# Performance work log

Hardware: AMD Instinct MI355X
Metric: run time of the kernel (lower is better)

The kernel has to match this reference:

```python
import jax, jax.numpy as jnp
import numpy as np

MIN_MARGIN = 0.15
MAX_MARGIN = 0.6
NUM_CALLS = 1  # first call; margin anneals over 40000 calls in the original
MARGIN = min(MIN_MARGIN + float(NUM_CALLS) / 40000.0 * (MAX_MARGIN - MIN_MARGIN), MAX_MARGIN)

B, C, D = 8192, 20000, 128


def setup_inputs() -> dict:
    key = jax.random.key(0)
    k1, k2, k3 = jax.random.split(key, 3)
    features = jax.random.normal(k1, (B, D), dtype=jnp.float32)
    centers = jax.random.normal(k2, (C, D), dtype=jnp.float32)
    labels = jax.random.randint(k3, (B,), 0, C, dtype=jnp.int64)
    return {"features": features, "centers": centers, "labels": labels}


def reference(features, centers, labels):
    # L2-normalize features along dim 1 (F.normalize default, eps=1e-12)
    norm = jnp.linalg.norm(features, axis=1, keepdims=True)
    f = features / jnp.maximum(norm, 1e-12)

    batch_centers = centers[labels]                       # [B, D]
    pos_distances = 1.0 - jnp.sum(f * batch_centers, axis=1)   # [B]
    neg_distances = 1.0 - jnp.einsum('bd,cd->bc', f, centers)  # [B, C]

    losses = MARGIN + pos_distances[:, None] - neg_distances   # [B, C]

    center_ids = jnp.arange(C, dtype=labels.dtype)
    different_class = labels[:, None] != center_ids[None, :]   # [B, C] bool
    valid = (different_class & (losses > 0.0)).astype(jnp.float32)

    num_valid = jnp.sum(valid)
    total = jnp.sum(losses * valid)
    return jnp.where(num_valid > 0, total / num_valid, jnp.zeros((), dtype=losses.dtype))
```

## Files before the change

kernel.cpp:

```cpp
#include <hip/hip_runtime.h>

#define B_N 8192
#define C_N 20000
#define D_N 128
#define CPAD 20096
#define NPAD 96
#define NTILES32 628
#define NCHUNK 24
#define MARGIN_F 0.15001125f

#define NORM_BLOCKS 1024
#define CONV_BLOCKS 2512

typedef __attribute__((ext_vector_type(8))) short bf16x8;
typedef __attribute__((ext_vector_type(4))) float f32x4;

typedef __attribute__((address_space(1))) const unsigned int GUint;
typedef __attribute__((address_space(3))) unsigned int LUint;

__device__ __forceinline__ unsigned short f2bf(float x) {
    union { float f; unsigned int u; } v; v.f = x;
    unsigned int r = v.u + 0x7fffu + ((v.u >> 16) & 1u);
    return (unsigned short)(r >> 16);
}
__device__ __forceinline__ float bf2f(unsigned short h) {
    union { unsigned int u; float f; } v; v.u = ((unsigned int)h) << 16; return v.f;
}

__global__ __launch_bounds__(256) void k_prep(
    const float* __restrict__ feat, const float* __restrict__ centers,
    const int* __restrict__ labels, unsigned short* __restrict__ fb,
    unsigned short* __restrict__ cb, float* __restrict__ t,
    float* __restrict__ corr_s, unsigned int* __restrict__ corr_c)
{
    const int bid = blockIdx.x;
    if (bid < NORM_BLOCKS) {
        const int lane = threadIdx.x & 63;
        const int l32  = lane & 31;
        const int row  = bid * 8 + ((threadIdx.x >> 6) << 1) + (lane >> 5);
        const float4 fv = *(const float4*)(feat + (size_t)row * D_N + l32 * 4);
        float ss = fv.x * fv.x + fv.y * fv.y + fv.z * fv.z + fv.w * fv.w;
        #pragma unroll
        for (int off = 16; off; off >>= 1) ss += __shfl_xor(ss, off);
        const float scale = 1.0f / fmaxf(sqrtf(ss), 1e-12f);
        const float a0 = fv.x * scale, a1 = fv.y * scale;
        const float a2 = fv.z * scale, a3 = fv.w * scale;
        ushort4 o; o.x = f2bf(a0); o.y = f2bf(a1); o.z = f2bf(a2); o.w = f2bf(a3);
        *(ushort4*)(fb + (size_t)row * D_N + l32 * 4) = o;

        const int lab = labels[row];
        const float4 cv = *(const float4*)(centers + (size_t)lab * D_N + l32 * 4);
        float pd = a0 * cv.x + a1 * cv.y + a2 * cv.z + a3 * cv.w;
        float pb = bf2f(o.x) * bf2f(f2bf(cv.x)) + bf2f(o.y) * bf2f(f2bf(cv.y))
                 + bf2f(o.z) * bf2f(f2bf(cv.z)) + bf2f(o.w) * bf2f(f2bf(cv.w));
        #pragma unroll
        for (int off = 16; off; off >>= 1) {
            pd += __shfl_xor(pd, off);
            pb += __shfl_xor(pb, off);
        }
        if (l32 == 0) {
            const float tb = MARGIN_F - pd;
            t[row] = tb;
            corr_s[row] = fmaxf(tb + pb, 0.0f) + (float)NPAD * fmaxf(tb, 0.0f);
            corr_c[row] = ((tb + pb > 0.0f) ? 1u : 0u) + ((tb > 0.0f) ? (unsigned)NPAD : 0u);
        }
    } else {
        const int idx = (bid - NORM_BLOCKS) * 256 + threadIdx.x;
        const int e = idx * 4;
        const int row = e >> 7;
        ushort4 o;
        if (row < C_N) {
            const float4 v = *(const float4*)(centers + e);
            o.x = f2bf(v.x); o.y = f2bf(v.y); o.z = f2bf(v.z); o.w = f2bf(v.w);
        } else {
            o.x = 0; o.y = 0; o.z = 0; o.w = 0;
        }
        *(ushort4*)(cb + e) = o;
    }
}

__global__ __launch_bounds__(256, 3) void k_main(
    const unsigned short* __restrict__ fb,
    const unsigned short* __restrict__ cb,
    const float* __restrict__ t,
    float* __restrict__ acc_slots)
{
    __shared__ __align__(16) unsigned short sB[2][32 * 128];
    __shared__ float sWsum[4];
    __shared__ unsigned int sWcnt[4];

    const int tid  = threadIdx.x;
    const int lane = tid & 63;
    const int w    = tid >> 6;
    const int chunk   = blockIdx.x;
    const int rowbase = blockIdx.y * 256;
    const int nt = (NTILES32 - 1 - chunk) / NCHUNK + 1;

    const int wf = w * 64;
    const int l15 = lane & 15;
    const int kg  = lane >> 4;

    bf16x8 ffr[4][4];
    float ntv[4];
    #pragma unroll
    for (int ff = 0; ff < 4; ++ff) {
        const int m = rowbase + wf + ff * 16 + l15;
        const unsigned short* src = fb + (size_t)m * D_N + kg * 8;
        #pragma unroll
        for (int ks = 0; ks < 4; ++ks)
            ffr[ks][ff] = *(const bf16x8*)(src + ks * 32);
        ntv[ff] = -t[m];
    }

    const f32x4 zero4 = {0.0f, 0.0f, 0.0f, 0.0f};

    const char* gB0 = (const char*)cb;
    auto STAGE = [&](int buf, int tile) {
        const char* gB = gB0 + (size_t)tile * 8192;
        #pragma unroll
        for (int i = 0; i < 2; ++i) {
            const int loff = w * 1024 + i * 4096;
            const int x = loff + lane * 16;
            const int sx = x ^ (((x >> 8) & 7) << 4);
            __builtin_amdgcn_global_load_lds((GUint*)(gB + sx),
                (LUint*)((char*)sB[buf] + loff), 16, 0, 0);
        }
    };

    STAGE(0, chunk);
    __syncthreads();

    float ls[4] = {0.0f, 0.0f, 0.0f, 0.0f};
    unsigned int wcnt = 0;

    for (int j = 0; j < nt; ++j) {
        const int cur = j & 1;
        if (j + 1 < nt) STAGE(cur ^ 1, chunk + (j + 1) * NCHUNK);

        const char* sbase = (const char*)sB[cur];
        f32x4 acc[2][4];
        #pragma unroll
        for (int ks = 0; ks < 4; ++ks) {
            bf16x8 cfr[2];
            #pragma unroll
            for (int fc = 0; fc < 2; ++fc) {
                const int row = fc * 16 + l15;
                int p = row * 256 + ks * 64 + kg * 16;
                p ^= ((row & 7) << 4);
                cfr[fc] = *(const bf16x8*)(sbase + p);
            }
            if (ks == 0) {
                #pragma unroll
                for (int fc = 0; fc < 2; ++fc)
                    #pragma unroll
                    for (int ff = 0; ff < 4; ++ff)
                        acc[fc][ff] = __builtin_amdgcn_mfma_f32_16x16x32_bf16(
                            cfr[fc], ffr[0][ff], zero4, 0, 0, 0);
            } else {
                #pragma unroll
                for (int fc = 0; fc < 2; ++fc)
                    #pragma unroll
                    for (int ff = 0; ff < 4; ++ff)
                        acc[fc][ff] = __builtin_amdgcn_mfma_f32_16x16x32_bf16(
                            cfr[fc], ffr[ks][ff], acc[fc][ff], 0, 0, 0);
            }
        }

        #pragma unroll
        for (int fc = 0; fc < 2; ++fc)
            #pragma unroll
            for (int ff = 0; ff < 4; ++ff)
                #pragma unroll
                for (int r = 0; r < 4; ++r) {
                    const float d = acc[fc][ff][r];
                    ls[fc * 2 + (ff & 1)] += fmaxf(d, ntv[ff]);
                    wcnt += (unsigned int)__popcll(__ballot(d > ntv[ff]));
                }

        __syncthreads();
    }

    float lsum = (ls[0] + ls[1]) + (ls[2] + ls[3]);
    #pragma unroll
    for (int off = 32; off; off >>= 1) lsum += __shfl_xor(lsum, off);
    if (lane == 0) { sWsum[w] = lsum; sWcnt[w] = wcnt; }
    __syncthreads();
    if (tid == 0) {
        float s = 0.0f; unsigned int c = 0;
        #pragma unroll
        for (int i = 0; i < 4; ++i) { s += sWsum[i]; c += sWcnt[i]; }
        const int slot = (blockIdx.x ^ blockIdx.y) & 3;
        atomicAdd(acc_slots + slot * 16, s);
        atomicAdd((unsigned int*)(acc_slots + slot * 16 + 1), c);
    }
}

__global__ __launch_bounds__(256) void k_finalize(
    const float* __restrict__ acc_slots, const float* __restrict__ t,
    const float* __restrict__ corr_s, const unsigned int* __restrict__ corr_c,
    float* __restrict__ out)
{
    __shared__ float ss[4], st[4];
    __shared__ unsigned int sc[4];
    const int tid = threadIdx.x;
    const int lane = tid & 63;
    const int w = tid >> 6;
    float cs = 0.0f, ct = 0.0f; unsigned int cc = 0;
    for (int i = tid; i < B_N; i += 256) {
        cs += corr_s[i]; ct += t[i]; cc += corr_c[i];
    }
    #pragma unroll
    for (int off = 32; off; off >>= 1) {
        cs += __shfl_xor(cs, off);
        ct += __shfl_xor(ct, off);
        cc += __shfl_xor(cc, off);
    }
    if (lane == 0) { ss[w] = cs; st[w] = ct; sc[w] = cc; }
    __syncthreads();
    if (tid == 0) {
        const double CS = (double)ss[0] + ss[1] + ss[2] + ss[3];
        const double CT = (double)st[0] + st[1] + st[2] + st[3];
        const long long CC = (long long)sc[0] + sc[1] + sc[2] + sc[3];
        double M = 0.0; long long Call = 0;
        #pragma unroll
        for (int i = 0; i < 4; ++i) {
            M += (double)acc_slots[i * 16];
            Call += (long long)((const unsigned int*)acc_slots)[i * 16 + 1];
        }
        const double S = M + (double)CPAD * CT - CS;
        const long long C = Call - CC;
        out[0] = (C > 0) ? (float)(S / (double)C) : 0.0f;
    }
}

extern "C" void kernel_launch(void* const* d_in, const int* in_sizes, int n_in,
                              void* d_out, int out_size, void* d_ws, size_t ws_size,
                              hipStream_t stream) {
    const float* feat    = (const float*)d_in[0];
    const float* centers = (const float*)d_in[1];
    const int*   labels  = (const int*)d_in[2];
    float* out = (float*)d_out;

    char* ws = (char*)d_ws;
    float*          acc_slots = (float*)ws;
    float*          t         = (float*)(ws + 1024);
    float*          corr_s    = (float*)(ws + 65536);
    unsigned int*   corr_c    = (unsigned int*)(ws + 98304);
    unsigned short* fb        = (unsigned short*)(ws + 131072);
    unsigned short* cb        = (unsigned short*)(ws + 4*1024*1024);

    hipMemsetAsync(ws, 0, 256, stream);
    k_prep<<<NORM_BLOCKS + CONV_BLOCKS, 256, 0, stream>>>(
        feat, centers, labels, fb, cb, t, corr_s, corr_c);
    dim3 grid(NCHUNK, 32);
    k_main<<<grid, 256, 0, stream>>>(fb, cb, t, acc_slots);
    k_finalize<<<1, 256, 0, stream>>>(acc_slots, t, corr_s, corr_c, out);
}
```

Before: 76.89 us.

## Software-pipeline MFMA with previous tile's epilogue using double accumulators

Uses two accumulator sets so that the max/ballot epilogue of tile j-1 is interleaved between the k-step MFMA groups of tile j, hiding VALU epilogue latency behind matrix-core work. It also preloads all four k-step LDS fragments up front. This doubles the accumulator register footprint and may raise register pressure and lower occupancy.

```diff
diff --git a/kernel.cpp b/kernel.cpp
--- a/kernel.cpp
+++ b/kernel.cpp
@@ -127,58 +127,88 @@
         }
     };
 
+    float ls[4] = {0.0f, 0.0f, 0.0f, 0.0f};
+    unsigned int wcnt = 0;
+
+    f32x4 accA[2][4], accB[2][4];
+
+#define EPI_SLICE(P, S)                                                 \
+    _Pragma("unroll")                                                   \
+    for (int fc = 0; fc < 2; ++fc)                                      \
+        _Pragma("unroll")                                               \
+        for (int r = 0; r < 4; ++r) {                                   \
+            const float d_ = P[fc][S][r];                               \
+            ls[fc * 2 + ((S) & 1)] += fmaxf(d_, ntv[S]);                \
+            wcnt += (unsigned int)__popcll(__ballot(d_ > ntv[S]));      \
+        }
+
+#define EPI_ALL(P) { EPI_SLICE(P, 0) EPI_SLICE(P, 1) EPI_SLICE(P, 2) EPI_SLICE(P, 3) }
+
+#define TILE_BODY(J, ACC, PREV, DO_EPI)                                 \
+    {                                                                   \
+        const int cur_ = (J) & 1;                                       \
+        if ((J) + 1 < nt) STAGE(cur_ ^ 1, chunk + ((J) + 1) * NCHUNK);  \
+        const char* sbase_ = (const char*)sB[cur_];                     \
+        bf16x8 cfr[4][2];                                               \
+        _Pragma("unroll")                                               \
+        for (int ks = 0; ks < 4; ++ks)                                  \
+            _Pragma("unroll")                                           \
+            for (int fc = 0; fc < 2; ++fc) {                            \
+                const int row_ = fc * 16 + l15;                         \
+                int p_ = row_ * 256 + ks * 64 + kg * 16;                \
+                p_ ^= ((row_ & 7) << 4);                                \
+                cfr[ks][fc] = *(const bf16x8*)(sbase_ + p_);            \
+            }                                                           \
+        _Pragma("unroll")                                               \
+        for (int fc = 0; fc < 2; ++fc)                                  \
+            _Pragma("unroll")                                           \
+            for (int ff = 0; ff < 4; ++ff)                              \
+                ACC[fc][ff] = __builtin_amdgcn_mfma_f32_16x16x32_bf16(  \
+                    cfr[0][fc], ffr[0][ff], zero4, 0, 0, 0);            \
+        if (DO_EPI) { EPI_SLICE(PREV, 0) }                              \
+        _Pragma("unroll")                                               \
+        for (int fc = 0; fc < 2; ++fc)                                  \
+            _Pragma("unroll")                                           \
+            for (int ff = 0; ff < 4; ++ff)                              \
+                ACC[fc][ff] = __builtin_amdgcn_mfma_f32_16x16x32_bf16(  \
+                    cfr[1][fc], ffr[1][ff], ACC[fc][ff], 0, 0, 0);      \
+        if (DO_EPI) { EPI_SLICE(PREV, 1) }                              \
+        _Pragma("unroll")                                               \
+        for (int fc = 0; fc < 2; ++fc)                                  \
+            _Pragma("unroll")                                           \
+            for (int ff = 0; ff < 4; ++ff)                              \
+                ACC[fc][ff] = __builtin_amdgcn_mfma_f32_16x16x32_bf16(  \
+                    cfr[2][fc], ffr[2][ff], ACC[fc][ff], 0, 0, 0);      \
+        if (DO_EPI) { EPI_SLICE(PREV, 2) }                              \
+        _Pragma("unroll")                                               \
+        for (int fc = 0; fc < 2; ++fc)                                  \
+            _Pragma("unroll")                                           \
+            for (int ff = 0; ff < 4; ++ff)                              \
+                ACC[fc][ff] = __builtin_amdgcn_mfma_f32_16x16x32_bf16(  \
+                    cfr[3][fc], ffr[3][ff], ACC[fc][ff], 0, 0, 0);      \
+        if (DO_EPI) { EPI_SLICE(PREV, 3) }                              \
+        __syncthreads();                                                \
+    }
+
     STAGE(0, chunk);
     __syncthreads();
 
-    float ls[4] = {0.0f, 0.0f, 0.0f, 0.0f};
-    unsigned int wcnt = 0;
-
-    for (int j = 0; j < nt; ++j) {
-        const int cur = j & 1;
-        if (j + 1 < nt) STAGE(cur ^ 1, chunk + (j + 1) * NCHUNK);
-
-        const char* sbase = (const char*)sB[cur];
-        f32x4 acc[2][4];
-        #pragma unroll
-        for (int ks = 0; ks < 4; ++ks) {
-            bf16x8 cfr[2];
-            #pragma unroll
-            for (int fc = 0; fc < 2; ++fc) {
-                const int row = fc * 16 + l15;
-                int p = row * 256 + ks * 64 + kg * 16;
-                p ^= ((row & 7) << 4);
-                cfr[fc] = *(const bf16x8*)(sbase + p);
-            }
-            if (ks == 0) {
-                #pragma unroll
-                for (int fc = 0; fc < 2; ++fc)
-                    #pragma unroll
-                    for (int ff = 0; ff < 4; ++ff)
-                        acc[fc][ff] = __builtin_amdgcn_mfma_f32_16x16x32_bf16(
-                            cfr[fc], ffr[0][ff], zero4, 0, 0, 0);
-            } else {
-                #pragma unroll
-                for (int fc = 0; fc < 2; ++fc)
-                    #pragma unroll
-                    for (int ff = 0; ff < 4; ++ff)
-                        acc[fc][ff] = __builtin_amdgcn_mfma_f32_16x16x32_bf16(
-                            cfr[fc], ffr[ks][ff], acc[fc][ff], 0, 0, 0);
-            }
-        }
-
-        #pragma unroll
-        for (int fc = 0; fc < 2; ++fc)
-            #pragma unroll
-            for (int ff = 0; ff < 4; ++ff)
-                #pragma unroll
-                for (int r = 0; r < 4; ++r) {
-                    const float d = acc[fc][ff][r];
-                    ls[fc * 2 + (ff & 1)] += fmaxf(d, ntv[ff]);
-                    wcnt += (unsigned int)__popcll(__ballot(d > ntv[ff]));
-                }
-
-        __syncthreads();
-    }
+    TILE_BODY(0, accA, accB, 0)
+    int j = 1;
+    for (; j + 1 < nt; j += 2) {
+        TILE_BODY(j,     accB, accA, 1)
+        TILE_BODY(j + 1, accA, accB, 1)
+    }
+    if (j < nt) {
+        TILE_BODY(j, accB, accA, 1)
+        EPI_ALL(accB)
+    } else {
+        EPI_ALL(accA)
+    }
+
+#undef TILE_BODY
+#undef EPI_ALL
+#undef EPI_SLICE
 
     float lsum = (ls[0] + ls[1]) + (ls[2] + ls[3]);
     #pragma unroll
```

Measured after the change: 78.80 us. 1.02x slower.
